# Kernel tuning notes

Measured on AMD Instinct MI355X. Metric: run time of the kernel, lower is better.

## Reference

```python
import jax, jax.numpy as jnp
import numpy as np

WS = 8          # window size
C = 192         # in_channels
NH = 4          # num_heads
QD = 16         # qkv_dim per head
HID = 16        # WindowBias hidden_dim = int(sqrt(64))*2
EPS = 1e-5


def _gen_bias_inputs():
    # Faithful replication of WindowBias._gen_input
    ys, xs = np.meshgrid(np.arange(WS), np.arange(WS), indexing='ij')
    pos = np.stack([ys, xs], axis=2).reshape(-1, 2)            # [N,2]
    N = pos.shape[0]
    delta = (pos[:, None, :] - pos[None, :, :]).reshape(N * N, 2)
    tuples = [tuple(d) for d in delta.tolist()]
    uniq = sorted(set(tuples))
    lut = {d: i for i, d in enumerate(uniq)}
    index = np.array([lut[d] for d in tuples], dtype=np.int64)  # [N*N]
    ud = np.array(uniq, dtype=np.float32)
    ud = ud / np.abs(ud).max()                                  # normalize by max |delta|
    return index, ud


def setup_inputs() -> dict:
    key = jax.random.key(0)
    ks = jax.random.split(key, 8)
    s = 0.02
    d = {}
    d['x'] = jax.random.normal(ks[0], (8, C, 192, 192), jnp.float32)
    d['ln_w'] = jnp.ones((C,), jnp.float32)                      # LayerNorm(bias=False) weight
    d['qkv_w'] = jax.random.normal(ks[1], (3 * NH * QD, C), jnp.float32) * s
    d['qkv_b'] = jnp.zeros((3 * NH * QD,), jnp.float32)
    d['proj_w'] = jax.random.normal(ks[2], (C, NH * QD), jnp.float32) * s
    d['proj_b'] = jnp.zeros((C,), jnp.float32)
    d['b1_w'] = jax.random.normal(ks[3], (HID, 2), jnp.float32) * s
    d['b1_b'] = jnp.zeros((HID,), jnp.float32)
    d['b2_w'] = jax.random.normal(ks[4], (1, HID), jnp.float32) * s
    d['b2_b'] = jnp.zeros((1,), jnp.float32)
    d['cw1'] = jax.random.normal(ks[5], (2 * C, C, 1, 1), jnp.float32) * s
    d['cb1'] = jnp.zeros((2 * C,), jnp.float32)
    d['cw2'] = jax.random.normal(ks[6], (C, C, 3, 3), jnp.float32) * s
    d['cb2'] = jnp.zeros((C,), jnp.float32)
    index, ud = _gen_bias_inputs()
    d['bias_index'] = jnp.asarray(index)   # [N*N] int64
    d['bias_delta'] = jnp.asarray(ud)      # [U,2] float32 (buffer, constant)
    return d


def reference(x, ln_w, qkv_w, qkv_b, proj_w, proj_b, b1_w, b1_b, b2_w, b2_b,
              cw1, cb1, cw2, cb2, bias_index, bias_delta):
    B, Cc, H, W = x.shape
    N = WS * WS
    nh, nw = H // WS, W // WS

    # --- relative position bias: tiny MLP + gather ---
    h = jax.nn.gelu(bias_delta @ b1_w.T + b1_b, approximate=False)
    bias = (h @ b2_w.T + b2_b)[:, 0][bias_index].reshape(N, N)

    # --- window partition: BCHW -> (B*nh*nw, N, C) ---
    xw = x.reshape(B, Cc, nh, WS, nw, WS).transpose(0, 2, 4, 3, 5, 1).reshape(-1, N, Cc)

    # --- pre-norm LayerNorm (no bias) ---
    mu = xw.mean(-1, keepdims=True)
    var = ((xw - mu) ** 2).mean(-1, keepdims=True)
    xn = (xw - mu) / jnp.sqrt(var + EPS) * ln_w

    # --- windowed MHA with additive relative bias ---
    qkv = xn @ qkv_w.T + qkv_b                                   # [Bw, N, 3*NH*QD]
    q, k, v = jnp.split(qkv, 3, axis=-1)
    heads = lambda t: t.reshape(-1, N, NH, QD).transpose(0, 2, 1, 3)  # [Bw, NH, N, QD]
    q, k, v = heads(q), heads(k), heads(v)
    scores = jnp.einsum('bhnd,bhmd->bhnm', q, k) / jnp.sqrt(jnp.float32(QD)) + bias
    attn = jax.nn.softmax(scores, axis=-1)
    o = jnp.einsum('bhnm,bhmd->bhnd', attn, v)
    o = o.transpose(0, 2, 1, 3).reshape(-1, N, NH * QD)
    o = o @ proj_w.T + proj_b                                    # [Bw, N, C]

    # --- window reverse: -> BCHW ---
    o = o.reshape(B, nh, nw, WS, WS, Cc).transpose(0, 5, 1, 3, 2, 4).reshape(B, Cc, H, W)
    x = x + o

    # --- conv GLU MLP: 1x1 -> GLU -> 3x3(replicate pad) -> LeakyReLU(0.1) ---
    y = jax.lax.conv_general_dilated(x, cw1, (1, 1), 'VALID') + cb1[None, :, None, None]
    a, b = jnp.split(y, 2, axis=1)
    y = a * jax.nn.sigmoid(b)
    yp = jnp.pad(y, ((0, 0), (0, 0), (1, 1), (1, 1)), mode='edge')
    y = jax.lax.conv_general_dilated(yp, cw2, (1, 1), 'VALID') + cb2[None, :, None, None]
    y = jnp.where(y >= 0, y, 0.1 * y)
    return x + y
```

## Files before the change

kernel.cpp:

```cpp
#include <hip/hip_runtime.h>
#include <hip/hip_bf16.h>
#include <math.h>

#define B_ 8
#define C_ 192
#define H_ 192
#define W_ 192
#define NWH 24

typedef __hip_bfloat16 bf16;
typedef short bf16x8 __attribute__((ext_vector_type(8)));
typedef short bf16x4 __attribute__((ext_vector_type(4)));
typedef float f32x4 __attribute__((ext_vector_type(4)));
typedef float f32x16 __attribute__((ext_vector_type(16)));

__device__ __forceinline__ float bf2f(bf16 v) { return __bfloat162float(v); }
__device__ __forceinline__ bf16 f2bf(float v) { return __float2bfloat16(v); }

union bu { bf16 b; ushort u; };

__device__ __forceinline__ uint packbf2(float a, float b) {
  bu c0, c1; c0.b = f2bf(a); c1.b = f2bf(b);
  return (uint)c0.u | ((uint)c1.u << 16);
}

__global__ __launch_bounds__(256) void k_prep(
    const float* __restrict__ b1_w, const float* __restrict__ b1_b,
    const float* __restrict__ b2_w, const float* __restrict__ b2_b,
    const int* __restrict__ bias_index, const float* __restrict__ bias_delta,
    const float* __restrict__ cw2,
    const float* __restrict__ ln_w, const float* __restrict__ qkv_w,
    float* __restrict__ bias_pk, bf16* __restrict__ wpk,
    float* __restrict__ rowsum) {
  int t = threadIdx.x;
  if (blockIdx.x == 0) {
    __shared__ float val[256];
    if (t < 225) {
      float dy = bias_delta[2 * t], dx = bias_delta[2 * t + 1];
      float acc = b2_b[0];
      for (int j = 0; j < 16; ++j) {
        float hj = b1_w[2 * j] * dy + b1_w[2 * j + 1] * dx + b1_b[j];
        float g = 0.5f * hj * (1.0f + erff(hj * 0.7071067811865475f));
        acc += g * b2_w[j];
      }
      val[t] = acc;
    }
    __syncthreads();
    for (int i = t; i < 4096; i += 256) {
      int idx = bias_index[i];
      idx = min(max(idx, 0), 224);
      float v = val[idx];
      int q = i >> 6, k = i & 63;
      int nt = q >> 5, m = k >> 5, kl = k & 31;
      int hi2 = (kl >> 2) & 1, reg = (kl & 3) + 4 * (kl >> 3);
      bias_pk[((nt * 2 + m) * 16 + reg) * 64 + (q & 31) + 32 * hi2] = v;
    }
  }
  if (blockIdx.x == 1 && t < 192) {
    float s = 0.f;
    for (int c = 0; c < C_; ++c) s += qkv_w[t * C_ + c] * ln_w[c];
    rowsum[t] = s;
  }
  int idx = blockIdx.x * 256 + t;
  if (idx < 9 * 192 * 192) {
    int tp = idx / 36864;
    int r = idx % 36864;
    int co = r / 192, ci = r % 192;
    wpk[idx] = f2bf(cw2[(co * 192 + ci) * 9 + tp]);
  }
}

__global__ __launch_bounds__(256) void k_ln_qkv(
    const float* __restrict__ x, const float* __restrict__ ln_w,
    const float* __restrict__ qkv_w, const float* __restrict__ qkv_b,
    const float* __restrict__ rowsum, bf16* __restrict__ qkv) {
  __shared__ ushort xs[64 * 204];
  __shared__ float red[512];
  __shared__ float mus[64], rsigs[64];
  int t = threadIdx.x;
  int blk = blockIdx.x;
  int b = blk / (H_ * 3);
  int rem = blk % (H_ * 3);
  int h = rem / 3;
  int w0 = (rem % 3) * 64;
  int p = t & 63, q = t >> 6;
  const float* xb = x + ((size_t)b * C_ * H_ + h) * W_ + w0;
  float s = 0.f, s2 = 0.f;
  for (int c = q; c < C_; c += 4) {
    float v = xb[(size_t)c * H_ * W_ + p];
    s += v; s2 += v * v;
    bu cv; cv.b = f2bf(v * ln_w[c]);
    xs[p * 204 + c] = cv.u;
  }
  red[q * 64 + p] = s;
  red[256 + q * 64 + p] = s2;
  __syncthreads();
  if (t < 64) {
    float su = red[t] + red[64 + t] + red[128 + t] + red[192 + t];
    float su2 = red[256 + t] + red[320 + t] + red[384 + t] + red[448 + t];
    float mu = su * (1.f / 192.f);
    float m2 = su2 * (1.f / 192.f);
    mus[t] = mu;
    rsigs[t] = rsqrtf(m2 - mu * mu + 1e-5f);
  }
  __syncthreads();

  int wave = t >> 6, lane = t & 63;
  int col16 = lane & 15, quad = lane >> 4;
  f32x4 acc[3][4];
#pragma unroll
  for (int mi = 0; mi < 3; ++mi)
#pragma unroll
    for (int ni = 0; ni < 4; ++ni)
#pragma unroll
      for (int r = 0; r < 4; ++r) acc[mi][ni][r] = 0.f;

  for (int ksi = 0; ksi < 6; ++ksi) {
    bf16x8 bfr[4];
#pragma unroll
    for (int ni = 0; ni < 4; ++ni) {
      const bf16x4* src =
          (const bf16x4*)(&xs[(ni * 16 + col16) * 204 + ksi * 32 + quad * 8]);
      union { bf16x8 v; bf16x4 h[2]; } u;
      u.h[0] = src[0];
      u.h[1] = src[1];
      bfr[ni] = u.v;
    }
#pragma unroll
    for (int mi = 0; mi < 3; ++mi) {
      int co = wave * 48 + mi * 16 + col16;
      const float* wsrc = qkv_w + (size_t)co * 192 + ksi * 32 + quad * 8;
      float4 wa = *(const float4*)(wsrc);
      float4 wb = *(const float4*)(wsrc + 4);
      bf16x8 a;
      {
        bu cv;
        cv.b = f2bf(wa.x); a[0] = (short)cv.u;
        cv.b = f2bf(wa.y); a[1] = (short)cv.u;
        cv.b = f2bf(wa.z); a[2] = (short)cv.u;
        cv.b = f2bf(wa.w); a[3] = (short)cv.u;
        cv.b = f2bf(wb.x); a[4] = (short)cv.u;
        cv.b = f2bf(wb.y); a[5] = (short)cv.u;
        cv.b = f2bf(wb.z); a[6] = (short)cv.u;
        cv.b = f2bf(wb.w); a[7] = (short)cv.u;
      }
#pragma unroll
      for (int ni = 0; ni < 4; ++ni)
        acc[mi][ni] =
            __builtin_amdgcn_mfma_f32_16x16x32_bf16(a, bfr[ni], acc[mi][ni], 0, 0, 0);
    }
  }

  size_t winbase = ((size_t)b * 24 + (h >> 3)) * 24 + (w0 >> 3);
  int hw8 = (h & 7) * 8;
  ushort* ob = (ushort*)qkv;
#pragma unroll
  for (int mi = 0; mi < 3; ++mi) {
    int cob = wave * 48 + mi * 16 + quad * 4;
#pragma unroll
    for (int r = 0; r < 4; ++r) {
      int co = cob + r;
      float rs = rowsum[co];
      float bv = qkv_b[co];
#pragma unroll
      for (int ni = 0; ni < 4; ++ni) {
        int px = ni * 16 + col16;
        float v = rsigs[px] * (acc[mi][ni][r] - mus[px] * rs) + bv;
        size_t off = ((winbase + (px >> 3)) * 192 + co) * 64 + hw8 + (px & 7);
        bu cv; cv.b = f2bf(v);
        ob[off] = cv.u;
      }
    }
  }
}

__global__ __launch_bounds__(256) void k_attn(
    const bf16* __restrict__ qkv, const float* __restrict__ bias_pk,
    const float* __restrict__ proj_w, const float* __restrict__ proj_b,
    const float* __restrict__ x, float* __restrict__ out) {
  __shared__ ushort qkvL[192 * 68];
  int t = threadIdx.x;
  int blk = blockIdx.x;
  int b = blk / (NWH * NWH);
  int rem = blk % (NWH * NWH);
  int wh = rem / NWH, ww = rem % NWH;
  int h0 = wh * 8, w0 = ww * 8;
  int lane = t & 63, hd = t >> 6;
  int l31 = lane & 31, hi = lane >> 5;
  int col16 = lane & 15, quad = lane >> 4;

  const ushort* qg = (const ushort*)qkv + (size_t)blk * 12288;
#pragma unroll
  for (int i = 0; i < 6; ++i) {
    int e = i * 256 + t;
    int ch = e >> 3, chunk = e & 7;
    uint4 v = *(const uint4*)(qg + ch * 64 + chunk * 8);
    ushort* dst = &qkvL[ch * 68 + chunk * 8];
    *(uint2*)dst = make_uint2(v.x, v.y);
    *(uint2*)(dst + 4) = make_uint2(v.z, v.w);
  }
  __syncthreads();

  bf16x8 ka[2], qb[2];
#pragma unroll
  for (int m = 0; m < 2; ++m) {
    union { bf16x8 v; ushort s[8]; } u;
#pragma unroll
    for (int j = 0; j < 8; ++j)
      u.s[j] = qkvL[(64 + hd * 16 + hi * 8 + j) * 68 + m * 32 + l31];
    ka[m] = u.v;
  }
#pragma unroll
  for (int n = 0; n < 2; ++n) {
    union { bf16x8 v; ushort s[8]; } u;
#pragma unroll
    for (int j = 0; j < 8; ++j)
      u.s[j] = qkvL[(hd * 16 + hi * 8 + j) * 68 + n * 32 + l31];
    qb[n] = u.v;
  }
  f32x16 accs[2][2];
#pragma unroll
  for (int m = 0; m < 2; ++m)
#pragma unroll
    for (int n = 0; n < 2; ++n) {
#pragma unroll
      for (int r = 0; r < 16; ++r) accs[m][n][r] = 0.f;
      accs[m][n] = __builtin_amdgcn_mfma_f32_32x32x16_bf16(ka[m], qb[n], accs[m][n], 0, 0, 0);
    }
  __syncthreads();

  uint pk[2][2][8];
#pragma unroll
  for (int nt = 0; nt < 2; ++nt) {
    float sc[2][16];
#pragma unroll
    for (int m = 0; m < 2; ++m)
#pragma unroll
      for (int r = 0; r < 16; ++r)
        sc[m][r] = fmaf(accs[m][nt][r], 0.25f,
                        bias_pk[((nt * 2 + m) * 16 + r) * 64 + lane]);
    float m8[8];
#pragma unroll
    for (int r = 0; r < 8; ++r)
      m8[r] = fmaxf(fmaxf(sc[0][r], sc[0][r + 8]), fmaxf(sc[1][r], sc[1][r + 8]));
    float mx = fmaxf(fmaxf(fmaxf(m8[0], m8[1]), fmaxf(m8[2], m8[3])),
                     fmaxf(fmaxf(m8[4], m8[5]), fmaxf(m8[6], m8[7])));
    mx = fmaxf(mx, __shfl_xor(mx, 32));
    float s8[8];
#pragma unroll
    for (int r = 0; r < 8; ++r) {
      float e0 = __expf(sc[0][r] - mx);      sc[0][r] = e0;
      float e1 = __expf(sc[0][r + 8] - mx);  sc[0][r + 8] = e1;
      float e2 = __expf(sc[1][r] - mx);      sc[1][r] = e2;
      float e3 = __expf(sc[1][r + 8] - mx);  sc[1][r + 8] = e3;
      s8[r] = (e0 + e1) + (e2 + e3);
    }
    float sum = ((s8[0] + s8[1]) + (s8[2] + s8[3])) + ((s8[4] + s8[5]) + (s8[6] + s8[7]));
    sum += __shfl_xor(sum, 32);
    float inv = 1.f / sum;
#pragma unroll
    for (int m = 0; m < 2; ++m)
#pragma unroll
      for (int rp = 0; rp < 8; ++rp)
        pk[nt][m][rp] = packbf2(sc[m][2 * rp] * inv, sc[m][2 * rp + 1] * inv);
  }

  f32x16 acco[2];
#pragma unroll
  for (int mt = 0; mt < 2; ++mt) {
#pragma unroll
    for (int r = 0; r < 16; ++r) acco[mt][r] = 0.f;
    uint sw[2][8];
#pragma unroll
    for (int mb = 0; mb < 2; ++mb)
#pragma unroll
      for (int rp = 0; rp < 8; ++rp)
        sw[mb][rp] = __shfl_xor(pk[mt][mb][rp], 32);
#pragma unroll
    for (int kc = 0; kc < 4; ++kc) {
      int mb = kc >> 1, r0 = (kc & 1) * 4;
      union { bf16x8 v; uint d[4]; } af;
      af.d[0] = hi ? sw[mb][r0 + 2] : pk[mt][mb][r0 + 0];
      af.d[1] = hi ? sw[mb][r0 + 3] : pk[mt][mb][r0 + 1];
      af.d[2] = hi ? pk[mt][mb][r0 + 2] : sw[mb][r0 + 0];
      af.d[3] = hi ? pk[mt][mb][r0 + 3] : sw[mb][r0 + 1];
      union { bf16x8 v; uint2 h[2]; } bv;
      const ushort* vsrc = &qkvL[(128 + hd * 16 + col16) * 68 + kc * 16 + hi * 8];
      bv.h[0] = *(const uint2*)(vsrc);
      bv.h[1] = *(const uint2*)(vsrc + 4);
      acco[mt] = __builtin_amdgcn_mfma_f32_32x32x16_bf16(af.v, bv.v, acco[mt], 0, 0, 0);
    }
  }
  if (l31 < 16) {
#pragma unroll
    for (int mt = 0; mt < 2; ++mt)
#pragma unroll
      for (int r = 0; r < 16; ++r) {
        int qrow = mt * 32 + (r & 3) + 8 * (r >> 2) + 4 * hi;
        bu cv; cv.b = f2bf(acco[mt][r]);
        qkvL[qrow * 68 + hd * 16 + l31] = cv.u;
      }
  }
  __syncthreads();

  f32x4 accp[3][4];
#pragma unroll
  for (int mi = 0; mi < 3; ++mi)
#pragma unroll
    for (int r = 0; r < 4; ++r) {
      float bv = proj_b[hd * 48 + mi * 16 + quad * 4 + r];
#pragma unroll
      for (int ni = 0; ni < 4; ++ni) accp[mi][ni][r] = bv;
    }
#pragma unroll
  for (int kc = 0; kc < 2; ++kc) {
    bf16x8 bos[4];
#pragma unroll
    for (int ni = 0; ni < 4; ++ni) {
      const ushort* src = &qkvL[(ni * 16 + col16) * 68 + kc * 32 + quad * 8];
      union { bf16x8 v; uint2 h[2]; } u;
      u.h[0] = *(const uint2*)(src);
      u.h[1] = *(const uint2*)(src + 4);
      bos[ni] = u.v;
    }
#pragma unroll
    for (int mi = 0; mi < 3; ++mi) {
      const float* wsrc = proj_w + (size_t)(hd * 48 + mi * 16 + col16) * 64 + kc * 32 + quad * 8;
      float4 wa = *(const float4*)(wsrc);
      float4 wb = *(const float4*)(wsrc + 4);
      bf16x8 a;
      {
        bu cv;
        cv.b = f2bf(wa.x); a[0] = (short)cv.u;
        cv.b = f2bf(wa.y); a[1] = (short)cv.u;
        cv.b = f2bf(wa.z); a[2] = (short)cv.u;
        cv.b = f2bf(wa.w); a[3] = (short)cv.u;
        cv.b = f2bf(wb.x); a[4] = (short)cv.u;
        cv.b = f2bf(wb.y); a[5] = (short)cv.u;
        cv.b = f2bf(wb.z); a[6] = (short)cv.u;
        cv.b = f2bf(wb.w); a[7] = (short)cv.u;
      }
#pragma unroll
      for (int ni = 0; ni < 4; ++ni)
        accp[mi][ni] = __builtin_amdgcn_mfma_f32_16x16x32_bf16(a, bos[ni], accp[mi][ni], 0, 0, 0);
    }
  }
  size_t base = ((size_t)b * C_ * H_ + h0) * W_ + w0;
#pragma unroll
  for (int mi = 0; mi < 3; ++mi) {
#pragma unroll
    for (int ni = 0; ni < 4; ++ni) {
#pragma unroll
      for (int r = 0; r < 4; ++r) {
        int co = hd * 48 + mi * 16 + quad * 4 + r;
        int px = ni * 16 + col16;
        size_t off = base + (size_t)co * H_ * W_ + (size_t)(px >> 3) * W_ + (px & 7);
        out[off] = accp[mi][ni][r] + x[off];
      }
    }
  }
}

__global__ __launch_bounds__(256) void k_conv1_glu(
    const float* __restrict__ xa, const float* __restrict__ cw1,
    const float* __restrict__ cb1, bf16* __restrict__ y) {
  __shared__ ushort xs[64 * 204];
  int t = threadIdx.x;
  int blk = blockIdx.x;
  int b = blk / (H_ * 3);
  int rem = blk % (H_ * 3);
  int h = rem / 3;
  int w0 = (rem % 3) * 64;
  int p = t & 63, q = t >> 6;
  const float* xb = xa + ((size_t)b * C_ * H_ + h) * W_ + w0;
  for (int c = q; c < C_; c += 4) {
    bu cv; cv.b = f2bf(xb[(size_t)c * H_ * W_ + p]);
    xs[p * 204 + c] = cv.u;
  }
  __syncthreads();

  int wave = t >> 6, lane = t & 63;
  int col16 = lane & 15, quad = lane >> 4;
  f32x4 acc[6][4];
#pragma unroll
  for (int mi = 0; mi < 6; ++mi) {
    int cob = (mi < 3) ? wave * 48 + mi * 16 : 192 + wave * 48 + (mi - 3) * 16;
#pragma unroll
    for (int r = 0; r < 4; ++r) {
      float bv = cb1[cob + quad * 4 + r];
#pragma unroll
      for (int ni = 0; ni < 4; ++ni) acc[mi][ni][r] = bv;
    }
  }

  for (int ksi = 0; ksi < 6; ++ksi) {
    bf16x8 bfr[4];
#pragma unroll
    for (int ni = 0; ni < 4; ++ni) {
      const bf16x4* src =
          (const bf16x4*)(&xs[(ni * 16 + col16) * 204 + ksi * 32 + quad * 8]);
      union { bf16x8 v; bf16x4 h[2]; } u;
      u.h[0] = src[0];
      u.h[1] = src[1];
      bfr[ni] = u.v;
    }
#pragma unroll
    for (int mi = 0; mi < 6; ++mi) {
      int cob = (mi < 3) ? wave * 48 + mi * 16 : 192 + wave * 48 + (mi - 3) * 16;
      const float* wsrc = cw1 + (size_t)(cob + col16) * 192 + ksi * 32 + quad * 8;
      float4 wa = *(const float4*)(wsrc);
      float4 wb = *(const float4*)(wsrc + 4);
      bf16x8 a;
      {
        bu cv;
        cv.b = f2bf(wa.x); a[0] = (short)cv.u;
        cv.b = f2bf(wa.y); a[1] = (short)cv.u;
        cv.b = f2bf(wa.z); a[2] = (short)cv.u;
        cv.b = f2bf(wa.w); a[3] = (short)cv.u;
        cv.b = f2bf(wb.x); a[4] = (short)cv.u;
        cv.b = f2bf(wb.y); a[5] = (short)cv.u;
        cv.b = f2bf(wb.z); a[6] = (short)cv.u;
        cv.b = f2bf(wb.w); a[7] = (short)cv.u;
      }
#pragma unroll
      for (int ni = 0; ni < 4; ++ni)
        acc[mi][ni] =
            __builtin_amdgcn_mfma_f32_16x16x32_bf16(a, bfr[ni], acc[mi][ni], 0, 0, 0);
    }
  }
  __syncthreads();

#pragma unroll
  for (int mi = 0; mi < 3; ++mi) {
#pragma unroll
    for (int ni = 0; ni < 4; ++ni) {
      int px = ni * 16 + col16;
      int co = wave * 48 + mi * 16 + quad * 4;
#pragma unroll
      for (int rr = 0; rr < 2; ++rr) {
        float a0 = acc[mi][ni][rr * 2], a1 = acc[mi][ni][rr * 2 + 1];
        float g0 = acc[mi + 3][ni][rr * 2], g1 = acc[mi + 3][ni][rr * 2 + 1];
        float r0 = a0 / (1.f + __expf(-g0));
        float r1 = a1 / (1.f + __expf(-g1));
        bu c0, c1;
        c0.b = f2bf(r0); c1.b = f2bf(r1);
        *(uint*)(&xs[px * 204 + co + rr * 2]) = (uint)c0.u | ((uint)c1.u << 16);
      }
    }
  }
  __syncthreads();
  ushort* yb = (ushort*)y + (((size_t)b * H_ + h) * W_ + w0) * 192;
#pragma unroll
  for (int i = 0; i < 6; ++i) {
    int e = i * 256 + t;
    int px = e / 24, ch = e % 24;
    uint u0 = *(const uint*)(&xs[px * 204 + ch * 8]);
    uint u1 = *(const uint*)(&xs[px * 204 + ch * 8 + 2]);
    uint u2 = *(const uint*)(&xs[px * 204 + ch * 8 + 4]);
    uint u3 = *(const uint*)(&xs[px * 204 + ch * 8 + 6]);
    uint4 pkv; pkv.x = u0; pkv.y = u1; pkv.z = u2; pkv.w = u3;
    *(uint4*)(yb + (size_t)px * 192 + ch * 8) = pkv;
  }
}

__global__ __launch_bounds__(256) void k_conv2(
    const bf16* __restrict__ y, const bf16* __restrict__ wpk,
    const float* __restrict__ cb2, float* __restrict__ out) {
  __shared__ ushort yl[6 * 18 * 204];
  int t = threadIdx.x;
  int blk = blockIdx.x;
  int b = blk / (48 * 12);
  int rem = blk % (48 * 12);
  int h0 = (rem / 12) * 4;
  int w0 = (rem % 12) * 16;
  const ushort* yg = (const ushort*)y;
  for (int e = t; e < 108 * 48; e += 256) {
    int p = e / 48, c8 = e % 48;
    int prow = p / 18, pcol = p % 18;
    int gr = min(max(h0 - 1 + prow, 0), H_ - 1);
    int gc = min(max(w0 - 1 + pcol, 0), W_ - 1);
    *(float2*)(&yl[p * 204 + c8 * 4]) =
        *(const float2*)(yg + (((size_t)b * H_ + gr) * W_ + gc) * 192 + c8 * 4);
  }
  __syncthreads();
  int wave = t >> 6, lane = t & 63;
  int col16 = lane & 15, quad = lane >> 4;
  f32x4 acc[3][4];
#pragma unroll
  for (int mi = 0; mi < 3; ++mi) {
#pragma unroll
    for (int r = 0; r < 4; ++r) {
      float bv = cb2[(wave * 3 + mi) * 16 + quad * 4 + r];
#pragma unroll
      for (int ni = 0; ni < 4; ++ni) acc[mi][ni][r] = bv;
    }
  }
  const ushort* wq = (const ushort*)wpk;
  for (int tap = 0; tap < 9; ++tap) {
    int dy = tap / 3, dx = tap % 3;
#pragma unroll
    for (int ks = 0; ks < 6; ++ks) {
      bf16x8 a[3];
#pragma unroll
      for (int mi = 0; mi < 3; ++mi) {
        int co = (wave * 3 + mi) * 16 + col16;
        a[mi] = *(const bf16x8*)(wq + ((size_t)tap * 192 + co) * 192 + ks * 32 + quad * 8);
      }
      bf16x8 bfr[4];
#pragma unroll
      for (int ni = 0; ni < 4; ++ni) {
        int p = (ni + dy) * 18 + col16 + dx;
        const bf16x4* src = (const bf16x4*)(&yl[p * 204 + ks * 32 + quad * 8]);
        union { bf16x8 v; bf16x4 h[2]; } u;
        u.h[0] = src[0];
        u.h[1] = src[1];
        bfr[ni] = u.v;
      }
#pragma unroll
      for (int mi = 0; mi < 3; ++mi)
#pragma unroll
        for (int ni = 0; ni < 4; ++ni)
          acc[mi][ni] = __builtin_amdgcn_mfma_f32_16x16x32_bf16(a[mi], bfr[ni], acc[mi][ni], 0, 0, 0);
    }
  }
#pragma unroll
  for (int mi = 0; mi < 3; ++mi) {
#pragma unroll
    for (int ni = 0; ni < 4; ++ni) {
#pragma unroll
      for (int r = 0; r < 4; ++r) {
        int co = (wave * 3 + mi) * 16 + quad * 4 + r;
        size_t off = (((size_t)b * C_ + co) * H_ + (h0 + ni)) * W_ + w0 + col16;
        float v = acc[mi][ni][r];
        v = (v >= 0.f) ? v : 0.1f * v;
        out[off] = out[off] + v;
      }
    }
  }
}

extern "C" void kernel_launch(void* const* d_in, const int* in_sizes, int n_in,
                              void* d_out, int out_size, void* d_ws, size_t ws_size,
                              hipStream_t stream) {
  const float* x      = (const float*)d_in[0];
  const float* ln_w   = (const float*)d_in[1];
  const float* qkv_w  = (const float*)d_in[2];
  const float* qkv_b  = (const float*)d_in[3];
  const float* proj_w = (const float*)d_in[4];
  const float* proj_b = (const float*)d_in[5];
  const float* b1_w   = (const float*)d_in[6];
  const float* b1_b   = (const float*)d_in[7];
  const float* b2_w   = (const float*)d_in[8];
  const float* b2_b   = (const float*)d_in[9];
  const float* cw1    = (const float*)d_in[10];
  const float* cb1    = (const float*)d_in[11];
  const float* cw2    = (const float*)d_in[12];
  const float* cb2    = (const float*)d_in[13];
  const int*   bidx   = (const int*)d_in[14];
  const float* bdelta = (const float*)d_in[15];
  float* out = (float*)d_out;

  char* ws = (char*)d_ws;
  float* bias   = (float*)ws;
  bf16*  wpk    = (bf16*)(ws + 16384);
  float* rowsum = (float*)(ws + 16384 + 663552);
  bf16*  big    = (bf16*)(ws + 16384 + 663552 + 1024);

  hipLaunchKernelGGL(k_prep, dim3(1296), dim3(256), 0, stream,
                     b1_w, b1_b, b2_w, b2_b, bidx, bdelta, cw2, ln_w, qkv_w,
                     bias, wpk, rowsum);
  hipLaunchKernelGGL(k_ln_qkv, dim3(4608), dim3(256), 0, stream,
                     x, ln_w, qkv_w, qkv_b, rowsum, big);
  hipLaunchKernelGGL(k_attn, dim3(4608), dim3(256), 0, stream,
                     big, bias, proj_w, proj_b, x, out);
  hipLaunchKernelGGL(k_conv1_glu, dim3(4608), dim3(256), 0, stream,
                     out, cw1, cb1, big);
  hipLaunchKernelGGL(k_conv2, dim3(4608), dim3(256), 0, stream,
                     big, wpk, cb2, out);
}
```

Before: 1.535 ms.

## Pre-convert weights to bf16 in prep kernel and double-buffer conv2 operand loads

The prep kernel now converts qkv_w, cw1 and proj_w to bf16 once, so the QKV, attention-projection and conv1 kernels load packed bf16 fragments directly instead of loading fp32 and converting in every block. The 3x3 conv kernel's tap and k-step loop is flattened and software-pipelined with two register buffers, so the next weight and shared-memory loads are issued before the current MFMAs run. This halves weight load bytes and removes the per-block conversion instructions. The cost is more register pressure from the duplicate operand buffers and extra workspace for the converted weights.

Measured after the change: 1.445 ms. 5.9% less time.

```diff
diff --git a/kernel.cpp b/kernel.cpp
--- a/kernel.cpp
+++ b/kernel.cpp
@@ -30,8 +30,11 @@
     const int* __restrict__ bias_index, const float* __restrict__ bias_delta,
     const float* __restrict__ cw2,
     const float* __restrict__ ln_w, const float* __restrict__ qkv_w,
+    const float* __restrict__ cw1, const float* __restrict__ proj_w,
     float* __restrict__ bias_pk, bf16* __restrict__ wpk,
-    float* __restrict__ rowsum) {
+    float* __restrict__ rowsum,
+    bf16* __restrict__ qkv_wb, bf16* __restrict__ cw1b,
+    bf16* __restrict__ projwb) {
   int t = threadIdx.x;
   if (blockIdx.x == 0) {
     __shared__ float val[256];
@@ -68,11 +71,14 @@
     int co = r / 192, ci = r % 192;
     wpk[idx] = f2bf(cw2[(co * 192 + ci) * 9 + tp]);
   }
+  if (idx < 36864) qkv_wb[idx] = f2bf(qkv_w[idx]);
+  if (idx < 73728) cw1b[idx] = f2bf(cw1[idx]);
+  if (idx < 12288) projwb[idx] = f2bf(proj_w[idx]);
 }
 
 __global__ __launch_bounds__(256) void k_ln_qkv(
     const float* __restrict__ x, const float* __restrict__ ln_w,
-    const float* __restrict__ qkv_w, const float* __restrict__ qkv_b,
+    const bf16* __restrict__ qkv_wb, const float* __restrict__ qkv_b,
     const float* __restrict__ rowsum, bf16* __restrict__ qkv) {
   __shared__ ushort xs[64 * 204];
   __shared__ float red[512];
@@ -115,6 +121,7 @@
 #pragma unroll
       for (int r = 0; r < 4; ++r) acc[mi][ni][r] = 0.f;
 
+  const ushort* wqv = (const ushort*)qkv_wb;
   for (int ksi = 0; ksi < 6; ++ksi) {
     bf16x8 bfr[4];
 #pragma unroll
@@ -129,21 +136,7 @@
 #pragma unroll
     for (int mi = 0; mi < 3; ++mi) {
       int co = wave * 48 + mi * 16 + col16;
-      const float* wsrc = qkv_w + (size_t)co * 192 + ksi * 32 + quad * 8;
-      float4 wa = *(const float4*)(wsrc);
-      float4 wb = *(const float4*)(wsrc + 4);
-      bf16x8 a;
-      {
-        bu cv;
-        cv.b = f2bf(wa.x); a[0] = (short)cv.u;
-        cv.b = f2bf(wa.y); a[1] = (short)cv.u;
-        cv.b = f2bf(wa.z); a[2] = (short)cv.u;
-        cv.b = f2bf(wa.w); a[3] = (short)cv.u;
-        cv.b = f2bf(wb.x); a[4] = (short)cv.u;
-        cv.b = f2bf(wb.y); a[5] = (short)cv.u;
-        cv.b = f2bf(wb.z); a[6] = (short)cv.u;
-        cv.b = f2bf(wb.w); a[7] = (short)cv.u;
-      }
+      bf16x8 a = *(const bf16x8*)(wqv + (size_t)co * 192 + ksi * 32 + quad * 8);
 #pragma unroll
       for (int ni = 0; ni < 4; ++ni)
         acc[mi][ni] =
@@ -176,7 +169,7 @@
 
 __global__ __launch_bounds__(256) void k_attn(
     const bf16* __restrict__ qkv, const float* __restrict__ bias_pk,
-    const float* __restrict__ proj_w, const float* __restrict__ proj_b,
+    const bf16* __restrict__ projwb, const float* __restrict__ proj_b,
     const float* __restrict__ x, float* __restrict__ out) {
   __shared__ ushort qkvL[192 * 68];
   int t = threadIdx.x;
@@ -312,6 +305,7 @@
 #pragma unroll
       for (int ni = 0; ni < 4; ++ni) accp[mi][ni][r] = bv;
     }
+  const ushort* wpj = (const ushort*)projwb;
 #pragma unroll
   for (int kc = 0; kc < 2; ++kc) {
     bf16x8 bos[4];
@@ -325,21 +319,8 @@
     }
 #pragma unroll
     for (int mi = 0; mi < 3; ++mi) {
-      const float* wsrc = proj_w + (size_t)(hd * 48 + mi * 16 + col16) * 64 + kc * 32 + quad * 8;
-      float4 wa = *(const float4*)(wsrc);
-      float4 wb = *(const float4*)(wsrc + 4);
-      bf16x8 a;
-      {
-        bu cv;
-        cv.b = f2bf(wa.x); a[0] = (short)cv.u;
-        cv.b = f2bf(wa.y); a[1] = (short)cv.u;
-        cv.b = f2bf(wa.z); a[2] = (short)cv.u;
-        cv.b = f2bf(wa.w); a[3] = (short)cv.u;
-        cv.b = f2bf(wb.x); a[4] = (short)cv.u;
-        cv.b = f2bf(wb.y); a[5] = (short)cv.u;
-        cv.b = f2bf(wb.z); a[6] = (short)cv.u;
-        cv.b = f2bf(wb.w); a[7] = (short)cv.u;
-      }
+      bf16x8 a = *(const bf16x8*)(wpj + (size_t)(hd * 48 + mi * 16 + col16) * 64 +
+                                  kc * 32 + quad * 8);
 #pragma unroll
       for (int ni = 0; ni < 4; ++ni)
         accp[mi][ni] = __builtin_amdgcn_mfma_f32_16x16x32_bf16(a, bos[ni], accp[mi][ni], 0, 0, 0);
@@ -362,7 +343,7 @@
 }
 
 __global__ __launch_bounds__(256) void k_conv1_glu(
-    const float* __restrict__ xa, const float* __restrict__ cw1,
+    const float* __restrict__ xa, const bf16* __restrict__ cw1b,
     const float* __restrict__ cb1, bf16* __restrict__ y) {
   __shared__ ushort xs[64 * 204];
   int t = threadIdx.x;
@@ -393,6 +374,7 @@
     }
   }
 
+  const ushort* wc1 = (const ushort*)cw1b;
   for (int ksi = 0; ksi < 6; ++ksi) {
     bf16x8 bfr[4];
 #pragma unroll
@@ -407,21 +389,7 @@
 #pragma unroll
     for (int mi = 0; mi < 6; ++mi) {
       int cob = (mi < 3) ? wave * 48 + mi * 16 : 192 + wave * 48 + (mi - 3) * 16;
-      const float* wsrc = cw1 + (size_t)(cob + col16) * 192 + ksi * 32 + quad * 8;
-      float4 wa = *(const float4*)(wsrc);
-      float4 wb = *(const float4*)(wsrc + 4);
-      bf16x8 a;
-      {
-        bu cv;
-        cv.b = f2bf(wa.x); a[0] = (short)cv.u;
-        cv.b = f2bf(wa.y); a[1] = (short)cv.u;
-        cv.b = f2bf(wa.z); a[2] = (short)cv.u;
-        cv.b = f2bf(wa.w); a[3] = (short)cv.u;
-        cv.b = f2bf(wb.x); a[4] = (short)cv.u;
-        cv.b = f2bf(wb.y); a[5] = (short)cv.u;
-        cv.b = f2bf(wb.z); a[6] = (short)cv.u;
-        cv.b = f2bf(wb.w); a[7] = (short)cv.u;
-      }
+      bf16x8 a = *(const bf16x8*)(wc1 + (size_t)(cob + col16) * 192 + ksi * 32 + quad * 8);
 #pragma unroll
       for (int ni = 0; ni < 4; ++ni)
         acc[mi][ni] =
@@ -496,32 +464,50 @@
     }
   }
   const ushort* wq = (const ushort*)wpk;
-  for (int tap = 0; tap < 9; ++tap) {
+  int co0 = wave * 48 + col16;
+
+  auto loada = [&](int tap, int ks, bf16x8 (&dst)[3]) {
+#pragma unroll
+    for (int mi = 0; mi < 3; ++mi)
+      dst[mi] = *(const bf16x8*)(wq + ((size_t)tap * 192 + co0 + mi * 16) * 192 +
+                                 ks * 32 + quad * 8);
+  };
+  auto loadb = [&](int tap, int ks, bf16x8 (&dst)[4]) {
     int dy = tap / 3, dx = tap % 3;
 #pragma unroll
-    for (int ks = 0; ks < 6; ++ks) {
-      bf16x8 a[3];
-#pragma unroll
-      for (int mi = 0; mi < 3; ++mi) {
-        int co = (wave * 3 + mi) * 16 + col16;
-        a[mi] = *(const bf16x8*)(wq + ((size_t)tap * 192 + co) * 192 + ks * 32 + quad * 8);
-      }
-      bf16x8 bfr[4];
-#pragma unroll
-      for (int ni = 0; ni < 4; ++ni) {
-        int p = (ni + dy) * 18 + col16 + dx;
-        const bf16x4* src = (const bf16x4*)(&yl[p * 204 + ks * 32 + quad * 8]);
-        union { bf16x8 v; bf16x4 h[2]; } u;
-        u.h[0] = src[0];
-        u.h[1] = src[1];
-        bfr[ni] = u.v;
-      }
-#pragma unroll
-      for (int mi = 0; mi < 3; ++mi)
-#pragma unroll
-        for (int ni = 0; ni < 4; ++ni)
-          acc[mi][ni] = __builtin_amdgcn_mfma_f32_16x16x32_bf16(a[mi], bfr[ni], acc[mi][ni], 0, 0, 0);
-    }
+    for (int ni = 0; ni < 4; ++ni) {
+      int p = (ni + dy) * 18 + col16 + dx;
+      const bf16x4* src = (const bf16x4*)(&yl[p * 204 + ks * 32 + quad * 8]);
+      union { bf16x8 v; bf16x4 h[2]; } u;
+      u.h[0] = src[0];
+      u.h[1] = src[1];
+      dst[ni] = u.v;
+    }
+  };
+
+  bf16x8 aA[3], bA[4], aB[3], bB[4];
+  loada(0, 0, aA);
+  loadb(0, 0, bA);
+  int ntap = 0, nks = 1;
+  for (int it = 0; it < 54; it += 2) {
+    loada(ntap, nks, aB);
+    loadb(ntap, nks, bB);
+    ++nks; if (nks == 6) { nks = 0; ++ntap; }
+#pragma unroll
+    for (int mi = 0; mi < 3; ++mi)
+#pragma unroll
+      for (int ni = 0; ni < 4; ++ni)
+        acc[mi][ni] = __builtin_amdgcn_mfma_f32_16x16x32_bf16(aA[mi], bA[ni], acc[mi][ni], 0, 0, 0);
+    if (it + 2 < 54) {
+      loada(ntap, nks, aA);
+      loadb(ntap, nks, bA);
+      ++nks; if (nks == 6) { nks = 0; ++ntap; }
+    }
+#pragma unroll
+    for (int mi = 0; mi < 3; ++mi)
+#pragma unroll
+      for (int ni = 0; ni < 4; ++ni)
+        acc[mi][ni] = __builtin_amdgcn_mfma_f32_16x16x32_bf16(aB[mi], bB[ni], acc[mi][ni], 0, 0, 0);
   }
 #pragma unroll
   for (int mi = 0; mi < 3; ++mi) {
@@ -563,18 +549,21 @@
   char* ws = (char*)d_ws;
   float* bias   = (float*)ws;
   bf16*  wpk    = (bf16*)(ws + 16384);
-  float* rowsum = (float*)(ws + 16384 + 663552);
-  bf16*  big    = (bf16*)(ws + 16384 + 663552 + 1024);
+  float* rowsum = (float*)(ws + 679936);
+  bf16*  qkv_wb = (bf16*)(ws + 680960);
+  bf16*  cw1b   = (bf16*)(ws + 754688);
+  bf16*  projwb = (bf16*)(ws + 902144);
+  bf16*  big    = (bf16*)(ws + 926720);
 
   hipLaunchKernelGGL(k_prep, dim3(1296), dim3(256), 0, stream,
                      b1_w, b1_b, b2_w, b2_b, bidx, bdelta, cw2, ln_w, qkv_w,
-                     bias, wpk, rowsum);
+                     cw1, proj_w, bias, wpk, rowsum, qkv_wb, cw1b, projwb);
   hipLaunchKernelGGL(k_ln_qkv, dim3(4608), dim3(256), 0, stream,
-                     x, ln_w, qkv_w, qkv_b, rowsum, big);
+                     x, ln_w, qkv_wb, qkv_b, rowsum, big);
   hipLaunchKernelGGL(k_attn, dim3(4608), dim3(256), 0, stream,
-                     big, bias, proj_w, proj_b, x, out);
+                     big, bias, projwb, proj_b, x, out);
   hipLaunchKernelGGL(k_conv1_glu, dim3(4608), dim3(256), 0, stream,
-                     out, cw1, cb1, big);
+                     out, cw1b, cb1, big);
   hipLaunchKernelGGL(k_conv2, dim3(4608), dim3(256), 0, stream,
                      big, wpk, cb2, out);
 }
```
